# Kernel optimization log

Hardware: AMD Instinct MI355X
Metric: run time of the kernel (lower is better)

Reference implementation:

```python
import jax, jax.numpy as jnp
import numpy as np

HEIGHT = 480
K = 16
RADIUS = 5.0 / HEIGHT


def ball_query_idx(xy, radius, k):
    """pytorch3d-style ball_query on 2D points (t-channel is zeroed in the
    original, so 3D distance == 2D distance on (x, y)).
    Returns first-k (in point-index order) neighbor indices within radius;
    slots with no neighbor are filled with the query's own index (the
    module's `-1 -> self` replacement).  xy: [B, N, 2] -> idx: [B, N, k] int32."""
    B, N, _ = xy.shape
    sq = jnp.sum(xy * xy, axis=-1)  # [B, N]
    # d2[b, i, j] = ||xy[b,i] - xy[b,j]||^2, via GEMM (no [B,N,N,2] intermediate)
    d2 = sq[:, :, None] + sq[:, None, :] - 2.0 * jnp.einsum('bnd,bmd->bnm', xy, xy)
    within = d2 < radius * radius  # [B, N, N]
    ar = jnp.arange(N, dtype=jnp.int32)
    # key = j if within else N; k smallest keys == first k neighbors in index order
    keys = jnp.where(within, ar[None, None, :], N)
    neg_top, _ = jax.lax.top_k(-keys, k)  # k smallest keys, ascending after negate
    idx = -neg_top  # [B, N, k]
    self_idx = jnp.broadcast_to(ar[None, :, None], (B, N, k))
    return jnp.where(idx < N, idx, self_idx)


def knn_gather(x, idx):
    # x: [B, N, D], idx: [B, N, k] -> [B, N, k, D]
    return jax.vmap(lambda xb, ib: xb[ib])(x, idx)


def setup_inputs() -> dict:
    key = jax.random.key(0)
    k1, k2, k3 = jax.random.split(key, 3)
    B, N = 8, 4096
    out_ch = 64
    hid = out_ch * 2          # 128
    in_ch = K * 2             # 32
    xytp = jax.random.uniform(k1, (B, N, 4), dtype=jnp.float32)
    W1 = jax.random.normal(k2, (in_ch, hid), dtype=jnp.float32) / np.sqrt(in_ch)
    b1 = jnp.zeros((hid,), dtype=jnp.float32)
    W2 = jax.random.normal(k3, (hid, out_ch), dtype=jnp.float32) / np.sqrt(hid)
    b2 = jnp.zeros((out_ch,), dtype=jnp.float32)
    return {"xytp": xytp, "W1": W1, "b1": b1, "W2": W2, "b2": b2}


def reference(xytp, W1, b1, W2, b2):
    xy = xytp[..., 1:3]  # [B, N, 2]
    # ball query runs on detached coords in the original
    idx = ball_query_idx(jax.lax.stop_gradient(xy), RADIUS, K)  # [B, N, K]
    delta = xy[:, :, None, :] - knn_gather(xy, idx)  # [B, N, K, 2]
    B, N = delta.shape[:2]
    emb = delta.reshape(B, N, K * 2)  # [B, N, 2K]
    h = jax.nn.relu(emb @ W1 + b1)
    return h @ W2 + b2  # [B, N, out_channel]
```

## Files before the change

kernel.cpp:

```cpp
#include <hip/hip_runtime.h>

#define NB    8
#define NPTS  4096
#define KNN   16
#define GRID  64
#define NCELL (GRID * GRID)
#define CAP   16

#define POISON ((int)0xAAAAAAAAu)

#define R2F ((float)((5.0 / 480.0) * (5.0 / 480.0)))


#define WS_BUCKET 0x20000

__global__ __launch_bounds__(256) void k_bucket(
    const float4* __restrict__ xytp4, int* __restrict__ cnts,
    float4* __restrict__ bucket) {
#pragma clang fp contract(off)
  int g = blockIdx.x * 256 + threadIdx.x;
  int b = g >> 12, n = g & 4095;
  float4 P = xytp4[g];
  float x = P.y, y = P.z;
  float sq = x * x + y * y;
  int cx = min(GRID - 1, max(0, (int)(x * (float)GRID)));
  int cy = min(GRID - 1, max(0, (int)(y * (float)GRID)));
  int cell = b * NCELL + cy * GRID + cx;
  int pos = atomicAdd(&cnts[cell], 1) - POISON;
  if (pos >= 0 && pos < CAP)
    bucket[cell * CAP + pos] = make_float4(x, y, sq, __int_as_float(n));
}

__global__ __launch_bounds__(1024, 8) void k_qmlp(
    const float4* __restrict__ xytp4, const int* __restrict__ cnts,
    const float4* __restrict__ bucket, const float* __restrict__ W1,
    const float* __restrict__ b1, const float* __restrict__ W2,
    const float* __restrict__ b2, float* __restrict__ out) {
#pragma clang fp contract(off)
  __shared__ float qx[64], qy[64], qsq[64];
  __shared__ unsigned short lists[64 * 9 * CAP];
  __shared__ int cnt9[64 * 9];
  __shared__ unsigned short scand[64 * 24];
  __shared__ unsigned short idxls[64 * KNN];
  __shared__ __align__(16) float embs[64 * 36];
  __shared__ __align__(16) float hs[64 * 132];

  const int t = threadIdx.x;
  const int p = t & 63;
  const int qq = t >> 6;
  const int pbase = blockIdx.x * 64;
  const int bb = pbase & ~4095;
  const int b = pbase >> 12;

  if (t < 64) {
    float4 P = xytp4[pbase + t];
    float x = P.y, y = P.z;
    qx[t] = x; qy[t] = y;
    qsq[t] = x * x + y * y;
  }
  if (t < 64 * 9) cnt9[t] = 0;
  __syncthreads();

  if (qq < 9) {
    float xn = qx[p], yn = qy[p], sqn = qsq[p];
    int cx = min(GRID - 1, max(0, (int)(xn * (float)GRID)));
    int cy = min(GRID - 1, max(0, (int)(yn * (float)GRID)));
    int row = cy + (qq / 3) - 1;
    int col = cx + (qq % 3) - 1;
    if (row >= 0 && row < GRID && col >= 0 && col < GRID) {
      int cell = b * NCELL + row * GRID + col;
      int cnt = min(max(cnts[cell] - POISON, 0), CAP);
      const float4* bk = bucket + cell * CAP;
      unsigned short* lst = &lists[(p * 9 + qq) * CAP];
      int c = 0;
      for (int i = 0; i < cnt; ++i) {
        float4 Q = bk[i];
        float tt = fmaf(yn, Q.y, xn * Q.x);
        float d = (sqn + Q.z) - (tt + tt);
        if (d < R2F) lst[c++] = (unsigned short)__float_as_int(Q.w);
      }
      cnt9[p * 9 + qq] = c;
    }
  }
  __syncthreads();

  if (t < 64) {
    unsigned short* cand = &scand[t * 24];
    int c = 0;
    for (int cc = 0; cc < 9; ++cc) {
      int rc = cnt9[t * 9 + cc];
      const unsigned short* lp = &lists[(t * 9 + cc) * CAP];
      for (int j = 0; j < rc && c < 24; ++j) cand[c++] = lp[j];
    }
    for (int i = 1; i < c; ++i) {
      unsigned short key = cand[i];
      int j = i - 1;
      while (j >= 0 && cand[j] > key) { cand[j + 1] = cand[j]; --j; }
      cand[j + 1] = key;
    }
    if (c > KNN) c = KNN;
    unsigned short selfI = (unsigned short)((pbase + t) & 4095);
    for (int k = 0; k < KNN; ++k)
      idxls[t * KNN + k] = (k < c) ? cand[k] : selfI;
  }
  __syncthreads();

  {
    int m = idxls[p * KNN + qq];
    float4 M = xytp4[bb + m];
    embs[p * 36 + 2 * qq] = qx[p] - M.y;
    embs[p * 36 + 2 * qq + 1] = qy[p] - M.z;
  }
  __syncthreads();

  {
    const int u0 = __builtin_amdgcn_readfirstlane(qq) * 8;
    float h[8];
#pragma unroll
    for (int j = 0; j < 8; ++j) h[j] = b1[u0 + j];
    const float4* er = (const float4*)&embs[p * 36];
#pragma unroll
    for (int g = 0; g < 8; ++g) {
      float4 e4 = er[g];
      const float* __restrict__ w0 = W1 + (4 * g) * 128 + u0;
#pragma unroll
      for (int j = 0; j < 8; ++j) h[j] = fmaf(e4.x, w0[j], h[j]);
#pragma unroll
      for (int j = 0; j < 8; ++j) h[j] = fmaf(e4.y, w0[128 + j], h[j]);
#pragma unroll
      for (int j = 0; j < 8; ++j) h[j] = fmaf(e4.z, w0[256 + j], h[j]);
#pragma unroll
      for (int j = 0; j < 8; ++j) h[j] = fmaf(e4.w, w0[384 + j], h[j]);
    }
    float* hr = &hs[p * 132 + u0];
    ((float4*)hr)[0] = make_float4(fmaxf(h[0], 0.f), fmaxf(h[1], 0.f),
                                   fmaxf(h[2], 0.f), fmaxf(h[3], 0.f));
    ((float4*)hr)[1] = make_float4(fmaxf(h[4], 0.f), fmaxf(h[5], 0.f),
                                   fmaxf(h[6], 0.f), fmaxf(h[7], 0.f));
  }
  __syncthreads();

  {
    const int o0 = __builtin_amdgcn_readfirstlane(qq) * 4;
    float acc[4];
#pragma unroll
    for (int j = 0; j < 4; ++j) acc[j] = b2[o0 + j];
    const float4* hv4 = (const float4*)&hs[p * 132];
#pragma unroll 4
    for (int g = 0; g < 32; ++g) {
      float4 hv = hv4[g];
      const float* __restrict__ w0 = W2 + (4 * g) * 64 + o0;
#pragma unroll
      for (int j = 0; j < 4; ++j) acc[j] = fmaf(hv.x, w0[j], acc[j]);
#pragma unroll
      for (int j = 0; j < 4; ++j) acc[j] = fmaf(hv.y, w0[64 + j], acc[j]);
#pragma unroll
      for (int j = 0; j < 4; ++j) acc[j] = fmaf(hv.z, w0[128 + j], acc[j]);
#pragma unroll
      for (int j = 0; j < 4; ++j) acc[j] = fmaf(hv.w, w0[192 + j], acc[j]);
    }
    *(float4*)(out + (size_t)(pbase + p) * 64 + o0) =
        make_float4(acc[0], acc[1], acc[2], acc[3]);
  }
}

extern "C" void kernel_launch(void* const* d_in, const int* in_sizes, int n_in,
                              void* d_out, int out_size, void* d_ws, size_t ws_size,
                              hipStream_t stream) {
  const float4* xytp4 = (const float4*)d_in[0];
  const float* W1 = (const float*)d_in[1];
  const float* b1 = (const float*)d_in[2];
  const float* W2 = (const float*)d_in[3];
  const float* b2 = (const float*)d_in[4];
  float* out = (float*)d_out;

  char* ws = (char*)d_ws;
  int* cnts = (int*)ws;
  float4* bucket = (float4*)(ws + WS_BUCKET);

  hipLaunchKernelGGL(k_bucket, dim3(128), dim3(256), 0, stream, xytp4, cnts,
                     bucket);
  hipLaunchKernelGGL(k_qmlp, dim3(512), dim3(1024), 0, stream, xytp4, cnts,
                     bucket, W1, b1, W2, b2, out);
}
```

Before: 89.47 us.

## Split fused query+MLP kernel into separate query and MLP kernels

The single fused kernel is split in two. A query kernel handles 16 points per 256-thread block and writes the gathered delta embeddings to a workspace buffer, and an MLP kernel reads them back. The query phase gets finer-grained blocks and better occupancy, and the MLP stores its hidden activations transposed in shared memory. In exchange there is an extra kernel launch and a global-memory round trip for the embeddings (about 4 MB).

```diff
diff --git a/kernel.cpp b/kernel.cpp
--- a/kernel.cpp
+++ b/kernel.cpp
@@ -11,8 +11,8 @@
 
 #define R2F ((float)((5.0 / 480.0) * (5.0 / 480.0)))
 
-
 #define WS_BUCKET 0x20000
+#define WS_EMB    0x820000
 
 __global__ __launch_bounds__(256) void k_bucket(
     const float4* __restrict__ xytp4, int* __restrict__ cnts,
@@ -31,60 +31,57 @@
     bucket[cell * CAP + pos] = make_float4(x, y, sq, __int_as_float(n));
 }
 
-__global__ __launch_bounds__(1024, 8) void k_qmlp(
+__global__ __launch_bounds__(256, 8) void k_query(
     const float4* __restrict__ xytp4, const int* __restrict__ cnts,
-    const float4* __restrict__ bucket, const float* __restrict__ W1,
-    const float* __restrict__ b1, const float* __restrict__ W2,
-    const float* __restrict__ b2, float* __restrict__ out) {
+    const float4* __restrict__ bucket, float2* __restrict__ emb2) {
 #pragma clang fp contract(off)
-  __shared__ float qx[64], qy[64], qsq[64];
-  __shared__ unsigned short lists[64 * 9 * CAP];
-  __shared__ int cnt9[64 * 9];
-  __shared__ unsigned short scand[64 * 24];
-  __shared__ unsigned short idxls[64 * KNN];
-  __shared__ __align__(16) float embs[64 * 36];
-  __shared__ __align__(16) float hs[64 * 132];
+  __shared__ float qx[16], qy[16], qsq[16];
+  __shared__ unsigned short lists[16 * 9 * CAP];
+  __shared__ int cnt9[16 * 9];
+  __shared__ unsigned short scand[16 * 24];
+  __shared__ unsigned short idxls[16 * KNN];
 
   const int t = threadIdx.x;
-  const int p = t & 63;
-  const int qq = t >> 6;
-  const int pbase = blockIdx.x * 64;
+  const int pbase = blockIdx.x * 16;
   const int bb = pbase & ~4095;
   const int b = pbase >> 12;
 
-  if (t < 64) {
+  if (t < 16) {
     float4 P = xytp4[pbase + t];
     float x = P.y, y = P.z;
     qx[t] = x; qy[t] = y;
     qsq[t] = x * x + y * y;
   }
-  if (t < 64 * 9) cnt9[t] = 0;
+  if (t < 16 * 9) cnt9[t] = 0;
   __syncthreads();
 
-  if (qq < 9) {
-    float xn = qx[p], yn = qy[p], sqn = qsq[p];
-    int cx = min(GRID - 1, max(0, (int)(xn * (float)GRID)));
-    int cy = min(GRID - 1, max(0, (int)(yn * (float)GRID)));
-    int row = cy + (qq / 3) - 1;
-    int col = cx + (qq % 3) - 1;
-    if (row >= 0 && row < GRID && col >= 0 && col < GRID) {
-      int cell = b * NCELL + row * GRID + col;
-      int cnt = min(max(cnts[cell] - POISON, 0), CAP);
-      const float4* bk = bucket + cell * CAP;
-      unsigned short* lst = &lists[(p * 9 + qq) * CAP];
-      int c = 0;
-      for (int i = 0; i < cnt; ++i) {
-        float4 Q = bk[i];
-        float tt = fmaf(yn, Q.y, xn * Q.x);
-        float d = (sqn + Q.z) - (tt + tt);
-        if (d < R2F) lst[c++] = (unsigned short)__float_as_int(Q.w);
+  {
+    const int p = t >> 4, c = t & 15;
+    if (c < 9) {
+      float xn = qx[p], yn = qy[p], sqn = qsq[p];
+      int cx = min(GRID - 1, max(0, (int)(xn * (float)GRID)));
+      int cy = min(GRID - 1, max(0, (int)(yn * (float)GRID)));
+      int row = cy + (c / 3) - 1;
+      int col = cx + (c % 3) - 1;
+      if (row >= 0 && row < GRID && col >= 0 && col < GRID) {
+        int cell = b * NCELL + row * GRID + col;
+        int cnt = min(max(cnts[cell] - POISON, 0), CAP);
+        const float4* bk = bucket + cell * CAP;
+        unsigned short* lst = &lists[(p * 9 + c) * CAP];
+        int cc = 0;
+        for (int i = 0; i < cnt; ++i) {
+          float4 Q = bk[i];
+          float tt = fmaf(yn, Q.y, xn * Q.x);
+          float d = (sqn + Q.z) - (tt + tt);
+          if (d < R2F) lst[cc++] = (unsigned short)__float_as_int(Q.w);
+        }
+        cnt9[p * 9 + c] = cc;
       }
-      cnt9[p * 9 + qq] = c;
     }
   }
   __syncthreads();
 
-  if (t < 64) {
+  if (t < 16) {
     unsigned short* cand = &scand[t * 24];
     int c = 0;
     for (int cc = 0; cc < 9; ++cc) {
@@ -106,19 +103,32 @@
   __syncthreads();
 
   {
-    int m = idxls[p * KNN + qq];
+    const int p = t >> 4, s = t & 15;
+    int m = idxls[p * KNN + s];
     float4 M = xytp4[bb + m];
-    embs[p * 36 + 2 * qq] = qx[p] - M.y;
-    embs[p * 36 + 2 * qq + 1] = qy[p] - M.z;
+    emb2[(size_t)(pbase + p) * 16 + s] =
+        make_float2(qx[p] - M.y, qy[p] - M.z);
   }
-  __syncthreads();
+}
+
+__global__ __launch_bounds__(1024, 8) void k_mlp(
+    const float4* __restrict__ emb4, const float* __restrict__ W1,
+    const float* __restrict__ b1, const float* __restrict__ W2,
+    const float* __restrict__ b2, float* __restrict__ out) {
+#pragma clang fp contract(off)
+  __shared__ float hsT[128][64];
+
+  const int t = threadIdx.x;
+  const int p = t & 63;
+  const int q = t >> 6;
+  const int pbase = blockIdx.x * 64;
 
   {
-    const int u0 = __builtin_amdgcn_readfirstlane(qq) * 8;
+    const int u0 = __builtin_amdgcn_readfirstlane(q) * 8;
     float h[8];
 #pragma unroll
     for (int j = 0; j < 8; ++j) h[j] = b1[u0 + j];
-    const float4* er = (const float4*)&embs[p * 36];
+    const float4* er = emb4 + (size_t)(pbase + p) * 8;
 #pragma unroll
     for (int g = 0; g < 8; ++g) {
       float4 e4 = er[g];
@@ -132,32 +142,25 @@
 #pragma unroll
       for (int j = 0; j < 8; ++j) h[j] = fmaf(e4.w, w0[384 + j], h[j]);
     }
-    float* hr = &hs[p * 132 + u0];
-    ((float4*)hr)[0] = make_float4(fmaxf(h[0], 0.f), fmaxf(h[1], 0.f),
-                                   fmaxf(h[2], 0.f), fmaxf(h[3], 0.f));
-    ((float4*)hr)[1] = make_float4(fmaxf(h[4], 0.f), fmaxf(h[5], 0.f),
-                                   fmaxf(h[6], 0.f), fmaxf(h[7], 0.f));
+#pragma unroll
+    for (int j = 0; j < 8; ++j) hsT[u0 + j][p] = fmaxf(h[j], 0.f);
   }
   __syncthreads();
 
   {
-    const int o0 = __builtin_amdgcn_readfirstlane(qq) * 4;
+    const int o0 = __builtin_amdgcn_readfirstlane(q) * 4;
     float acc[4];
 #pragma unroll
     for (int j = 0; j < 4; ++j) acc[j] = b2[o0 + j];
-    const float4* hv4 = (const float4*)&hs[p * 132];
 #pragma unroll 4
-    for (int g = 0; g < 32; ++g) {
-      float4 hv = hv4[g];
-      const float* __restrict__ w0 = W2 + (4 * g) * 64 + o0;
+    for (int g = 0; g < 64; ++g) {
+      float h0 = hsT[2 * g][p];
+      float h1 = hsT[2 * g + 1][p];
+      const float* __restrict__ w0 = W2 + (2 * g) * 64 + o0;
 #pragma unroll
-      for (int j = 0; j < 4; ++j) acc[j] = fmaf(hv.x, w0[j], acc[j]);
+      for (int j = 0; j < 4; ++j) acc[j] = fmaf(h0, w0[j], acc[j]);
 #pragma unroll
-      for (int j = 0; j < 4; ++j) acc[j] = fmaf(hv.y, w0[64 + j], acc[j]);
-#pragma unroll
-      for (int j = 0; j < 4; ++j) acc[j] = fmaf(hv.z, w0[128 + j], acc[j]);
-#pragma unroll
-      for (int j = 0; j < 4; ++j) acc[j] = fmaf(hv.w, w0[192 + j], acc[j]);
+      for (int j = 0; j < 4; ++j) acc[j] = fmaf(h1, w0[64 + j], acc[j]);
     }
     *(float4*)(out + (size_t)(pbase + p) * 64 + o0) =
         make_float4(acc[0], acc[1], acc[2], acc[3]);
@@ -177,9 +180,13 @@
   char* ws = (char*)d_ws;
   int* cnts = (int*)ws;
   float4* bucket = (float4*)(ws + WS_BUCKET);
+  float2* emb2 = (float2*)(ws + WS_EMB);
+  const float4* emb4 = (const float4*)(ws + WS_EMB);
 
   hipLaunchKernelGGL(k_bucket, dim3(128), dim3(256), 0, stream, xytp4, cnts,
                      bucket);
-  hipLaunchKernelGGL(k_qmlp, dim3(512), dim3(1024), 0, stream, xytp4, cnts,
-                     bucket, W1, b1, W2, b2, out);
+  hipLaunchKernelGGL(k_query, dim3(2048), dim3(256), 0, stream, xytp4, cnts,
+                     bucket, emb2);
+  hipLaunchKernelGGL(k_mlp, dim3(512), dim3(1024), 0, stream, emb4, W1, b1,
+                     W2, b2, out);
 }
```

New measurement: 96.33 us. +7.7%, slower.
